# Optimization experiments

Hardware: AMD Instinct MI355X
Metric: run time of the kernel (lower is better)

## Reference

```python
import jax, jax.numpy as jnp
import numpy as np

B, T, C, H, L, FFN = 2, 2048, 512, 4, 4, 2048
H = 8
KD = C // H          # key_dim = head_dim (value_factor=1)
SCALE = KD ** -0.5
EPS = 1e-6


def _gelu(x):
    return jax.nn.gelu(x, approximate=False)  # keras default gelu is exact


def _ln(x):
    m = jnp.mean(x, axis=-1, keepdims=True)
    v = jnp.mean((x - m) ** 2, axis=-1, keepdims=True)
    return (x - m) / jnp.sqrt(v + EPS)


def _rotate_every_two(x):
    x1 = x[..., ::2]
    x2 = x[..., 1::2]
    return jnp.stack((-x2, x1), axis=-1).reshape(x.shape)


def _theta_shift(x, sin, cos):
    # x: [B,H,T,KD]; sin/cos: [T,KD] broadcast over B,H
    return x * cos + _rotate_every_two(x) * sin


def _rel_pos():
    half = KD // 2
    angle = 1.0 / (10000.0 ** jnp.linspace(0.0, 1.0, half))
    angle = jnp.repeat(angle, 2)                       # interleaved duplicate -> [KD]
    idx = jnp.arange(T, dtype=jnp.float32)
    sin = jnp.sin(idx[:, None] * angle[None, :])       # [T,KD]
    cos = jnp.cos(idx[:, None] * angle[None, :])
    decay = jnp.log(1.0 - 2.0 ** (-5.0 - jnp.arange(H, dtype=jnp.float32)))  # [H]
    diff = idx[:, None] - idx[None, :]                 # [T,T]
    masked = jnp.where(diff >= 0, jnp.exp(diff * decay[:, None, None]), 0.0)  # [H,T,T]
    mask = masked / jnp.sqrt(jnp.sum(masked, axis=-1, keepdims=True))
    return sin, cos, mask


def _split_heads(t):
    # [B,T,C] -> [B,H,T,KD]
    return t.reshape(B, T, H, KD).transpose(0, 2, 1, 3)


def _retention(x, Wq, bq, Wk, bk, Wv, bv, Wg, bg, Wo, bo, sin, cos, mask):
    q = _gelu(x @ Wq + bq)
    k = _gelu(x @ Wk + bk) * SCALE
    v = _gelu(x @ Wv + bv)
    g = _gelu(x @ Wg + bg)
    qr = _theta_shift(_split_heads(q), sin, cos)
    kr = _theta_shift(_split_heads(k), sin, cos)
    vr = _split_heads(v)
    qk = jnp.einsum('bhtd,bhsd->bhts', qr, kr) * mask[None]
    ssum = jnp.clip(jnp.abs(jnp.sum(qk, axis=-1, keepdims=True)), 1.0, None)
    qk = qk / (ssum + EPS)
    out = jnp.einsum('bhts,bhsd->bhtd', qk, vr)
    out = out.transpose(0, 2, 1, 3).reshape(B, T, C)
    out = _ln(out)                                     # group_norm (LayerNormalization)
    out = (g * jax.nn.sigmoid(g)) * out                # swish gate
    return _gelu(out @ Wo + bo)


def setup_inputs() -> dict:
    key = jax.random.key(0)
    ks = jax.random.split(key, 8)
    s = 0.02
    d = {'x': jax.random.normal(ks[0], (B, T, C), jnp.float32)}
    d['Wq'] = jax.random.normal(ks[1], (L, C, C), jnp.float32) * s
    d['bq'] = jnp.zeros((L, C), jnp.float32)
    d['Wk'] = jax.random.normal(ks[2], (L, C, C), jnp.float32) * s
    d['bk'] = jnp.zeros((L, C), jnp.float32)
    d['Wv'] = jax.random.normal(ks[3], (L, C, C), jnp.float32) * s
    d['bv'] = jnp.zeros((L, C), jnp.float32)
    d['Wg'] = jax.random.normal(ks[4], (L, C, C), jnp.float32) * s
    d['bg'] = jnp.zeros((L, C), jnp.float32)
    d['Wo'] = jax.random.normal(ks[5], (L, C, C), jnp.float32) * s
    d['bo'] = jnp.zeros((L, C), jnp.float32)
    d['W1'] = jax.random.normal(ks[6], (L, C, FFN), jnp.float32) * s
    d['b1'] = jnp.zeros((L, FFN), jnp.float32)
    d['W2'] = jax.random.normal(ks[7], (L, FFN, C), jnp.float32) * s
    d['b2'] = jnp.zeros((L, C), jnp.float32)
    return d


def reference(x, Wq, bq, Wk, bk, Wv, bv, Wg, bg, Wo, bo, W1, b1, W2, b2):
    sin, cos, mask = _rel_pos()
    for l in range(L):
        # pre-norm retention block (normalize_before=True, alpha=1, dropout off)
        res = x
        h = _ln(x)
        h = _retention(h, Wq[l], bq[l], Wk[l], bk[l], Wv[l], bv[l],
                       Wg[l], bg[l], Wo[l], bo[l], sin, cos, mask)
        x = res + h
        # pre-norm FFN block with internal layernorm (use_ffn_layernorm=True)
        res = x
        h = _ln(x)
        h = _gelu(h @ W1[l] + b1[l])
        h = _ln(h)
        h = _gelu(h @ W2[l] + b2[l])
        x = res + h
    return x
```

## Files before the change

### kernel.cpp

```cpp
#include <hip/hip_runtime.h>
#include <math.h>

typedef __bf16 bf16_t;
typedef __bf16 bf16x4 __attribute__((ext_vector_type(4)));
typedef __bf16 bf16x8 __attribute__((ext_vector_type(8)));
typedef float f32x4 __attribute__((ext_vector_type(4)));

#define DEV __device__ __forceinline__

constexpr int Bc = 2, Tc = 2048, Cc = 512, Hc = 8, FFNc = 2048, Lc = 4;
constexpr int Mc = Bc * Tc;
constexpr float kSCALE = 0.125f;
constexpr float kEPS = 1e-6f;

constexpr size_t OFF_WQKVG = 0;
constexpr size_t OFF_WO    = OFF_WQKVG + (size_t)Lc*2048*512*2;
constexpr size_t OFF_W1    = OFF_WO    + (size_t)Lc*512*512*2;
constexpr size_t OFF_W2    = OFF_W1    + (size_t)Lc*2048*512*2;
constexpr size_t OFF_BQKVG = OFF_W2    + (size_t)Lc*512*2048*2;
constexpr size_t OFF_TABC  = OFF_BQKVG + (size_t)Lc*2048*4;
constexpr size_t OFF_TABS  = OFF_TABC  + (size_t)Tc*32*4;
constexpr size_t OFF_HLN   = OFF_TABS  + (size_t)Tc*32*4;
constexpr size_t OFF_QKVG  = OFF_HLN   + (size_t)Mc*2048*2;
constexpr size_t OFF_QR    = OFF_QKVG  + (size_t)Mc*2048*4;
constexpr size_t OFF_KR    = OFF_QR    + (size_t)Bc*Hc*Tc*64*2;
constexpr size_t OFF_VT    = OFF_KR    + (size_t)Bc*Hc*Tc*64*2;
constexpr size_t OFF_AO    = OFF_VT    + (size_t)Bc*Hc*64*Tc*2;
constexpr size_t OFF_GATED = OFF_AO    + (size_t)Mc*512*4;

DEV float gelu_f(float x) { return 0.5f * x * (1.0f + erff(x * 0.70710678118654752f)); }

DEV void async_load16(const void* g, void* l) {
  __builtin_amdgcn_global_load_lds((const __attribute__((address_space(1))) unsigned int*)g,
                                   (__attribute__((address_space(3))) unsigned int*)l, 16, 0, 0);
}

__global__ __launch_bounds__(256) void transpose_pack_k(const float* __restrict__ src, bf16_t* __restrict__ dst,
                                                        int K, int N, size_t src_lstride, size_t dst_lstride) {
  __shared__ float tile[32][33];
  src += blockIdx.z * src_lstride;
  dst += blockIdx.z * dst_lstride;
  const int n0 = blockIdx.x * 32, k0 = blockIdx.y * 32;
  const int tx = threadIdx.x, ty = threadIdx.y;
#pragma unroll
  for (int j = 0; j < 32; j += 8) tile[ty + j][tx] = src[(size_t)(k0 + ty + j) * N + n0 + tx];
  __syncthreads();
#pragma unroll
  for (int j = 0; j < 32; j += 8) dst[(size_t)(n0 + ty + j) * K + k0 + tx] = (bf16_t)tile[tx][ty + j];
}

__global__ __launch_bounds__(256) void biaspack_k(const float* __restrict__ bq, const float* __restrict__ bk,
                                                  const float* __restrict__ bv, const float* __restrict__ bg,
                                                  float* __restrict__ outp) {
  const int tid = blockIdx.x * 256 + threadIdx.x;
  const int l = tid >> 11, n = tid & 2047;
  const float* srcs[4] = {bq, bk, bv, bg};
  outp[tid] = srcs[n >> 9][l * 512 + (n & 511)];
}

__global__ __launch_bounds__(256) void trig_k(float* __restrict__ tc, float* __restrict__ ts) {
  const int tid = blockIdx.x * 256 + threadIdx.x;
  const int t = tid >> 5, i = tid & 31;
  const float angle = powf(10000.f, -(float)i / 31.f);
  const float a = (float)t * angle;
  tc[tid] = cosf(a);
  ts[tid] = sinf(a);
}

template <int NC>
__global__ __launch_bounds__(256) void ln_k(const float* __restrict__ in, bf16_t* __restrict__ out) {
  constexpr int PT = NC / 256;
  const int row = blockIdx.x;
  const float* rp = in + (size_t)row * NC;
  float v[PT], s = 0.f, sq = 0.f;
#pragma unroll
  for (int i = 0; i < PT; ++i) { v[i] = rp[threadIdx.x + i * 256]; s += v[i]; sq += v[i] * v[i]; }
#pragma unroll
  for (int m = 1; m < 64; m <<= 1) { s += __shfl_xor(s, m); sq += __shfl_xor(sq, m); }
  __shared__ float red[8];
  const int wave = threadIdx.x >> 6, lane = threadIdx.x & 63;
  if (lane == 0) { red[wave] = s; red[4 + wave] = sq; }
  __syncthreads();
  s = red[0] + red[1] + red[2] + red[3];
  sq = red[4] + red[5] + red[6] + red[7];
  const float mean = s * (1.f / NC);
  const float inv = rsqrtf(sq * (1.f / NC) - mean * mean + kEPS);
  bf16_t* op = out + (size_t)row * NC;
#pragma unroll
  for (int i = 0; i < PT; ++i) op[threadIdx.x + i * 256] = (bf16_t)((v[i] - mean) * inv);
}

template <int BM, int BN, int WM, int WN, int EPI>
__global__ __launch_bounds__(256) void gemm_k(const bf16_t* __restrict__ A, const bf16_t* __restrict__ Bt,
                                              const float* __restrict__ bias, const float* __restrict__ res,
                                              float* __restrict__ out, int M, int N, int K,
                                              const float* __restrict__ tabc, const float* __restrict__ tabs,
                                              bf16_t* __restrict__ qrp, bf16_t* __restrict__ krp,
                                              bf16_t* __restrict__ vtp) {
  constexpr int BK = 32;
  constexpr int WIN_M = WM / 16, WIN_N = WN / 16;
  __shared__ bf16_t lds[2][(BM + BN) * BK];
  const int wave = threadIdx.x >> 6, lane = threadIdx.x & 63;
  const int nwg = gridDim.x * gridDim.y;
  const int orig = blockIdx.y * gridDim.x + blockIdx.x;
  const int wg = (orig & 7) * (nwg >> 3) + (orig >> 3);
  const int bx = wg % gridDim.x, by = wg / gridDim.x;
  const int m0 = by * BM, n0 = bx * BN;
  const int wm = wave >> 1, wn = wave & 1;
  f32x4 acc[WIN_M][WIN_N] = {};
  const int lrow = lane >> 2, lcb = (lane & 3) * 8;
  const int ksub = (lane >> 4) * 8, rsub = lane & 15;

#define GSTAGE(bf_, kt_)                                                              \
  {                                                                                   \
    for (int i = wave; i < BM / 16; i += 4)                                           \
      async_load16(A + (size_t)(m0 + i * 16 + lrow) * K + (kt_) + lcb,                \
                   &lds[bf_][i * 16 * BK]);                                           \
    for (int i = wave; i < BN / 16; i += 4)                                           \
      async_load16(Bt + (size_t)(n0 + i * 16 + lrow) * K + (kt_) + lcb,               \
                   &lds[bf_][BM * BK + i * 16 * BK]);                                 \
  }

  int buf = 0;
  GSTAGE(0, 0);
  __syncthreads();
  for (int kt = 0; kt < K; kt += BK) {
    if (kt + BK < K) GSTAGE(buf ^ 1, kt + BK);
    const bf16_t* bufA = &lds[buf][0];
    const bf16_t* bufB = &lds[buf][BM * BK];
    bf16x8 af[WIN_M], bfr[WIN_N];
#pragma unroll
    for (int mi = 0; mi < WIN_M; ++mi) af[mi] = *(const bf16x8*)&bufA[(wm * WM + mi * 16 + rsub) * BK + ksub];
#pragma unroll
    for (int ni = 0; ni < WIN_N; ++ni) bfr[ni] = *(const bf16x8*)&bufB[(wn * WN + ni * 16 + rsub) * BK + ksub];
#pragma unroll
    for (int mi = 0; mi < WIN_M; ++mi)
#pragma unroll
      for (int ni = 0; ni < WIN_N; ++ni)
        acc[mi][ni] = __builtin_amdgcn_mfma_f32_16x16x32_bf16(af[mi], bfr[ni], acc[mi][ni], 0, 0, 0);
    __syncthreads();
    buf ^= 1;
  }
#undef GSTAGE

#pragma unroll
  for (int mi = 0; mi < WIN_M; ++mi)
#pragma unroll
    for (int ni = 0; ni < WIN_N; ++ni) {
      const int col = n0 + wn * WN + ni * 16 + (lane & 15);
      const int row0 = m0 + wm * WM + mi * 16 + (lane >> 4) * 4;
      const float bv = bias ? bias[col] : 0.f;
      if constexpr (EPI == 2) {
        const int region = col >> 9;
        if (region <= 1) {
          const int hh = (col >> 6) & 7, d = col & 63, ti = d >> 1;
          bf16_t* dst = region ? krp : qrp;
#pragma unroll
          for (int r = 0; r < 4; ++r) {
            float v = gelu_f(acc[mi][ni][r] + bv);
            if (region == 1) v *= kSCALE;
            const float p = __shfl_xor(v, 1);
            const int m = row0 + r, t = m & 2047, bb = m >> 11;
            const float cv = tabc[t * 32 + ti], sv = tabs[t * 32 + ti];
            const float rot = (d & 1) ? p : -p;
            dst[((size_t)((bb * 8 + hh) * 2048 + t)) * 64 + d] = (bf16_t)(v * cv + rot * sv);
          }
        } else if (region == 2) {
          const int hh = (col >> 6) & 7, d = col & 63;
          const int m = row0, t0 = m & 2047, bb = m >> 11;
          bf16x4 pk;
#pragma unroll
          for (int r = 0; r < 4; ++r) pk[r] = (bf16_t)gelu_f(acc[mi][ni][r] + bv);
          *(bf16x4*)&vtp[((size_t)((bb * 8 + hh) * 64 + d)) * 2048 + t0] = pk;
        } else {
#pragma unroll
          for (int r = 0; r < 4; ++r)
            out[(size_t)(row0 + r) * N + col] = gelu_f(acc[mi][ni][r] + bv);
        }
      } else {
#pragma unroll
        for (int r = 0; r < 4; ++r) {
          float v = gelu_f(acc[mi][ni][r] + bv);
          if constexpr (EPI == 3) v += res[(size_t)(row0 + r) * N + col];
          out[(size_t)(row0 + r) * N + col] = v;
        }
      }
    }
}

__global__ __launch_bounds__(512) void retention_k(const bf16_t* __restrict__ qr, const bf16_t* __restrict__ kr,
                                                   const bf16_t* __restrict__ vt, float* __restrict__ ao) {
  const int bid = blockIdx.x;
  const int j = bid >> 3;
  const int bh = (bid & 7) * 2 + (j & 1);
  const int qp = j >> 1;
  const int h = bh & 7, b = bh >> 3;
  const int wave = threadIdx.x >> 6, lane = threadIdx.x & 63;
  const int sub = wave & 3, half = wave >> 2;
  const int gi = lane >> 4, li = lane & 15;
  const float dec = log1pf(-exp2f(-5.f - (float)h));
  const float d2 = dec * 1.44269504088896340736f;
  const float inv1md = exp2f(5.f + (float)h);
  __shared__ bf16_t kv[2][2][2][64][64];
  __shared__ bf16_t sS[8][16][76];
  __shared__ float red[4][64][21];
  const size_t base = (size_t)bh * (size_t)Tc * 64;
  const bf16_t* vbh = vt + (size_t)bh * 64 * Tc;

  const int srow = lane >> 3;
  const int schunk = (lane & 7) ^ srow;
  const int roff0 = li * 64 + (((gi) ^ (li & 7)) << 3);
  const int roff1 = li * 64 + (((gi + 4) ^ (li & 7)) << 3);

  float bS[4];
#pragma unroll
  for (int sc = 0; sc < 4; ++sc) bS[sc] = exp2f(-d2 * (float)(sc * 16 + li));

#define STAGE(bf_, st_)                                                                   \
  {                                                                                       \
    const bf16_t* kt_ = kr + base + (size_t)(st_) * 64 * 64;                              \
    const bf16_t* vt_ = vbh + (st_) * 64;                                                 \
    _Pragma("unroll") for (int jj = 0; jj < 2; ++jj) {                                    \
      const int rb_ = sub * 2 + jj;                                                       \
      async_load16(kt_ + (size_t)(rb_ * 8 + srow) * 64 + schunk * 8, &kv[bf_][half][0][rb_ * 8][0]); \
      async_load16(vt_ + (size_t)(rb_ * 8 + srow) * Tc + schunk * 8, &kv[bf_][half][1][rb_ * 8][0]); \
    }                                                                                     \
  }

  for (int part = 0; part < 2; ++part) {
    const int q = part ? (31 - qp) : qp;
    const int tw = q * 64 + sub * 16;
    bf16x8 qf0, qf1;
    {
      const bf16_t* qptr = qr + base + (size_t)(tw + li) * 64 + gi * 8;
      qf0 = *(const bf16x8*)qptr;
      qf1 = *(const bf16x8*)(qptr + 32);
    }
    f32x4 accv[4] = {};
    float rs[4] = {0.f, 0.f, 0.f, 0.f};

    const int nsteps = (q + 2) >> 1;
    int buf = 0;
    if (half <= q) STAGE(0, half);
    __syncthreads();
    for (int i = 0; i < nsteps; ++i) {
      const int st = 2 * i + half;
      const int stn = st + 2;
      if (stn <= q) STAGE(buf ^ 1, stn);
      if (st <= q) {
        const int s0g = st * 64;
        const bf16_t* kb = &kv[buf][half][0][0][0];
        const bf16_t* vb = &kv[buf][half][1][0][0];
        float aT[4];
#pragma unroll
        for (int r = 0; r < 4; ++r) aT[r] = exp2f(d2 * (float)(tw + gi * 4 + r - s0g));
#pragma unroll
        for (int sc = 0; sc < 4; ++sc) {
          const bf16x8 kf0 = *(const bf16x8*)(kb + sc * 16 * 64 + roff0);
          const bf16x8 kf1 = *(const bf16x8*)(kb + sc * 16 * 64 + roff1);
          f32x4 Sv = {};
          Sv = __builtin_amdgcn_mfma_f32_16x16x32_bf16(qf0, kf0, Sv, 0, 0, 0);
          Sv = __builtin_amdgcn_mfma_f32_16x16x32_bf16(qf1, kf1, Sv, 0, 0, 0);
          const int s_l = sc * 16 + li;
#pragma unroll
          for (int r = 0; r < 4; ++r) {
            const float w = (s0g + s_l <= tw + gi * 4 + r) ? aT[r] * bS[sc] : 0.f;
            const float val = Sv[r] * w;
            rs[r] += val;
            sS[wave][gi * 4 + r][s_l] = (bf16_t)val;
          }
        }
        const bf16x8 pa0 = *(const bf16x8*)&sS[wave][li][gi * 8];
        const bf16x8 pa1 = *(const bf16x8*)&sS[wave][li][32 + gi * 8];
#pragma unroll
        for (int dd = 0; dd < 4; ++dd) {
          const bf16x8 vb0 = *(const bf16x8*)(vb + dd * 16 * 64 + roff0);
          const bf16x8 vb1 = *(const bf16x8*)(vb + dd * 16 * 64 + roff1);
          accv[dd] = __builtin_amdgcn_mfma_f32_16x16x32_bf16(pa0, vb0, accv[dd], 0, 0, 0);
          accv[dd] = __builtin_amdgcn_mfma_f32_16x16x32_bf16(pa1, vb1, accv[dd], 0, 0, 0);
        }
      }
      __syncthreads();
      buf ^= 1;
    }

#pragma unroll
    for (int r = 0; r < 4; ++r) {
      float v = rs[r];
      v += __shfl_xor(v, 1); v += __shfl_xor(v, 2); v += __shfl_xor(v, 4); v += __shfl_xor(v, 8);
      rs[r] = v;
    }
    if (half == 1) {
      float* rp = red[sub][lane];
#pragma unroll
      for (int dd = 0; dd < 4; ++dd)
#pragma unroll
        for (int r = 0; r < 4; ++r) rp[dd * 4 + r] = accv[dd][r];
#pragma unroll
      for (int r = 0; r < 4; ++r) rp[16 + r] = rs[r];
    }
    __syncthreads();
    if (half == 0) {
      const float* rp = red[sub][lane];
#pragma unroll
      for (int r = 0; r < 4; ++r) {
        const int t = tw + gi * 4 + r;
        const float Ssum = -expm1f(dec * (float)(t + 1)) * inv1md;
        const float rt = rsqrtf(Ssum);
        const float rsv = rs[r] + rp[16 + r];
        const float den = fmaxf(fabsf(rsv * rt), 1.0f) + kEPS;
        const float scl = rt / den;
        float* op = ao + ((size_t)(b * Tc + t)) * Cc + h * 64 + li;
#pragma unroll
        for (int dd = 0; dd < 4; ++dd) op[dd * 16] = (accv[dd][r] + rp[dd * 4 + r]) * scl;
      }
    }
    __syncthreads();
  }
#undef STAGE
}

__global__ __launch_bounds__(256) void postret_k(const float* __restrict__ ao, const float* __restrict__ qkvg,
                                                 bf16_t* __restrict__ gated) {
  const int row = blockIdx.x;
  const float* rp = ao + (size_t)row * 512;
  float v0 = rp[threadIdx.x], v1 = rp[threadIdx.x + 256];
  float s = v0 + v1, sq = v0 * v0 + v1 * v1;
#pragma unroll
  for (int m = 1; m < 64; m <<= 1) { s += __shfl_xor(s, m); sq += __shfl_xor(sq, m); }
  __shared__ float red[8];
  const int wave = threadIdx.x >> 6, lane = threadIdx.x & 63;
  if (lane == 0) { red[wave] = s; red[4 + wave] = sq; }
  __syncthreads();
  s = red[0] + red[1] + red[2] + red[3];
  sq = red[4] + red[5] + red[6] + red[7];
  const float mean = s * (1.f / 512.f);
  const float inv = rsqrtf(sq * (1.f / 512.f) - mean * mean + kEPS);
  const float* gp = qkvg + (size_t)row * 2048 + 1536;
  const float g0 = gp[threadIdx.x], g1 = gp[threadIdx.x + 256];
  bf16_t* op = gated + (size_t)row * 512;
  op[threadIdx.x] = (bf16_t)(g0 / (1.f + expf(-g0)) * (v0 - mean) * inv);
  op[threadIdx.x + 256] = (bf16_t)(g1 / (1.f + expf(-g1)) * (v1 - mean) * inv);
}

extern "C" void kernel_launch(void* const* d_in, const int* in_sizes, int n_in,
                              void* d_out, int out_size, void* d_ws, size_t ws_size,
                              hipStream_t stream) {
  const float* x_in = (const float*)d_in[0];
  const float* Wq = (const float*)d_in[1];
  const float* bq = (const float*)d_in[2];
  const float* Wk = (const float*)d_in[3];
  const float* bk = (const float*)d_in[4];
  const float* Wv = (const float*)d_in[5];
  const float* bv = (const float*)d_in[6];
  const float* Wg = (const float*)d_in[7];
  const float* bg = (const float*)d_in[8];
  const float* Wo = (const float*)d_in[9];
  const float* bo = (const float*)d_in[10];
  const float* W1 = (const float*)d_in[11];
  const float* b1 = (const float*)d_in[12];
  const float* W2 = (const float*)d_in[13];
  const float* b2 = (const float*)d_in[14];

  char* ws = (char*)d_ws;
  bf16_t* WQKVG = (bf16_t*)(ws + OFF_WQKVG);
  bf16_t* WOt   = (bf16_t*)(ws + OFF_WO);
  bf16_t* W1t   = (bf16_t*)(ws + OFF_W1);
  bf16_t* W2t   = (bf16_t*)(ws + OFF_W2);
  float*  BQKVG = (float*)(ws + OFF_BQKVG);
  float*  TABC  = (float*)(ws + OFF_TABC);
  float*  TABS  = (float*)(ws + OFF_TABS);
  bf16_t* HLN   = (bf16_t*)(ws + OFF_HLN);
  float*  QKVG  = (float*)(ws + OFF_QKVG);
  bf16_t* QR    = (bf16_t*)(ws + OFF_QR);
  bf16_t* KR    = (bf16_t*)(ws + OFF_KR);
  bf16_t* VT    = (bf16_t*)(ws + OFF_VT);
  float*  AO    = (float*)(ws + OFF_AO);
  bf16_t* GATED = (bf16_t*)(ws + OFF_GATED);
  float*  xbuf  = (float*)d_out;

  hipMemcpyAsync(xbuf, x_in, (size_t)Mc * Cc * 4, hipMemcpyDeviceToDevice, stream);

  const dim3 tb(32, 8);
  const float* wsrc[4] = {Wq, Wk, Wv, Wg};
  for (int c = 0; c < 4; ++c)
    transpose_pack_k<<<dim3(Cc / 32, Cc / 32, Lc), tb, 0, stream>>>(
        wsrc[c], WQKVG + (size_t)c * Cc * Cc, Cc, Cc, (size_t)Cc * Cc, (size_t)2048 * Cc);
  transpose_pack_k<<<dim3(Cc / 32, Cc / 32, Lc), tb, 0, stream>>>(
      Wo, WOt, Cc, Cc, (size_t)Cc * Cc, (size_t)Cc * Cc);
  transpose_pack_k<<<dim3(FFNc / 32, Cc / 32, Lc), tb, 0, stream>>>(
      W1, W1t, Cc, FFNc, (size_t)Cc * FFNc, (size_t)FFNc * Cc);
  transpose_pack_k<<<dim3(Cc / 32, FFNc / 32, Lc), tb, 0, stream>>>(
      W2, W2t, FFNc, Cc, (size_t)FFNc * Cc, (size_t)Cc * FFNc);
  biaspack_k<<<32, 256, 0, stream>>>(bq, bk, bv, bg, BQKVG);
  trig_k<<<256, 256, 0, stream>>>(TABC, TABS);

  for (int l = 0; l < Lc; ++l) {
    ln_k<512><<<Mc, 256, 0, stream>>>(xbuf, HLN);
    gemm_k<64, 128, 32, 64, 2><<<dim3(2048 / 128, Mc / 64), 256, 0, stream>>>(
        HLN, WQKVG + (size_t)l * 2048 * 512, BQKVG + l * 2048, nullptr, QKVG, Mc, 2048, 512,
        TABC, TABS, QR, KR, VT);
    retention_k<<<256, 512, 0, stream>>>(QR, KR, VT, AO);
    postret_k<<<Mc, 256, 0, stream>>>(AO, QKVG, GATED);
    gemm_k<64, 64, 32, 32, 3><<<dim3(512 / 64, Mc / 64), 256, 0, stream>>>(
        GATED, WOt + (size_t)l * 512 * 512, bo + l * 512, xbuf, xbuf, Mc, 512, 512,
        nullptr, nullptr, nullptr, nullptr, nullptr);
    ln_k<512><<<Mc, 256, 0, stream>>>(xbuf, HLN);
    gemm_k<64, 128, 32, 64, 1><<<dim3(2048 / 128, Mc / 64), 256, 0, stream>>>(
        HLN, W1t + (size_t)l * 2048 * 512, b1 + l * 2048, nullptr, QKVG, Mc, 2048, 512,
        nullptr, nullptr, nullptr, nullptr, nullptr);
    ln_k<2048><<<Mc, 256, 0, stream>>>(QKVG, HLN);
    gemm_k<64, 64, 32, 32, 3><<<dim3(512 / 64, Mc / 64), 256, 0, stream>>>(
        HLN, W2t + (size_t)l * 512 * 2048, b2 + l * 512, xbuf, xbuf, Mc, 512, 2048,
        nullptr, nullptr, nullptr, nullptr, nullptr);
  }
}
```

Measured before the change: 696.5 us.

## Use triple-buffered LDS with vmcnt waits and single barrier per k-step

Switches the GEMM and retention main loops from double-buffered LDS with two __syncthreads per step to a three-slot ring. Each step issues the next tile's async loads unconditionally (clamped to a valid tile), then uses s_waitcnt vmcnt(N) plus one s_barrier so only the current tile must have landed. The goal is to cut barrier count and keep global-to-LDS loads in flight across the MFMA work. It costs 50% more LDS, which may lower occupancy, and adds redundant loads at the tail; correctness depends on the vmcnt count matching the number of loads each wave issues per stage.

Measured after the change: 675.7 us. 1.03x faster.

```diff
diff --git a/kernel.cpp b/kernel.cpp
--- a/kernel.cpp
+++ b/kernel.cpp
@@ -35,6 +35,11 @@
                                    (__attribute__((address_space(3))) unsigned int*)l, 16, 0, 0);
 }
 
+#define PIPE_WAIT_BARRIER(J_)                                        \
+  asm volatile("s_waitcnt vmcnt(%0)" ::"i"(J_) : "memory");          \
+  __builtin_amdgcn_s_barrier();                                      \
+  __builtin_amdgcn_sched_barrier(0);
+
 __global__ __launch_bounds__(256) void transpose_pack_k(const float* __restrict__ src, bf16_t* __restrict__ dst,
                                                         int K, int N, size_t src_lstride, size_t dst_lstride) {
   __shared__ float tile[32][33];
@@ -99,7 +104,8 @@
                                               bf16_t* __restrict__ vtp) {
   constexpr int BK = 32;
   constexpr int WIN_M = WM / 16, WIN_N = WN / 16;
-  __shared__ bf16_t lds[2][(BM + BN) * BK];
+  constexpr int JL = (BM + BN) / 64;
+  __shared__ bf16_t lds[3][(BM + BN) * BK];
   const int wave = threadIdx.x >> 6, lane = threadIdx.x & 63;
   const int nwg = gridDim.x * gridDim.y;
   const int orig = blockIdx.y * gridDim.x + blockIdx.x;
@@ -121,13 +127,14 @@
                    &lds[bf_][BM * BK + i * 16 * BK]);                                 \
   }
 
-  int buf = 0;
+  const int NT = K / BK;
   GSTAGE(0, 0);
-  __syncthreads();
-  for (int kt = 0; kt < K; kt += BK) {
-    if (kt + BK < K) GSTAGE(buf ^ 1, kt + BK);
-    const bf16_t* bufA = &lds[buf][0];
-    const bf16_t* bufB = &lds[buf][BM * BK];
+  for (int tt = 0; tt < NT; ++tt) {
+    const int ktn = (tt + 1 < NT) ? (tt + 1) * BK : (NT - 1) * BK;
+    GSTAGE((tt + 1) % 3, ktn);
+    PIPE_WAIT_BARRIER(JL);
+    const bf16_t* bufA = &lds[tt % 3][0];
+    const bf16_t* bufB = &lds[tt % 3][BM * BK];
     bf16x8 af[WIN_M], bfr[WIN_N];
 #pragma unroll
     for (int mi = 0; mi < WIN_M; ++mi) af[mi] = *(const bf16x8*)&bufA[(wm * WM + mi * 16 + rsub) * BK + ksub];
@@ -138,10 +145,9 @@
 #pragma unroll
       for (int ni = 0; ni < WIN_N; ++ni)
         acc[mi][ni] = __builtin_amdgcn_mfma_f32_16x16x32_bf16(af[mi], bfr[ni], acc[mi][ni], 0, 0, 0);
-    __syncthreads();
-    buf ^= 1;
   }
 #undef GSTAGE
+  asm volatile("s_waitcnt vmcnt(0)" ::: "memory");
 
 #pragma unroll
   for (int mi = 0; mi < WIN_M; ++mi)
@@ -201,7 +207,7 @@
   const float dec = log1pf(-exp2f(-5.f - (float)h));
   const float d2 = dec * 1.44269504088896340736f;
   const float inv1md = exp2f(5.f + (float)h);
-  __shared__ bf16_t kv[2][2][2][64][64];
+  __shared__ bf16_t kv[3][2][2][64][64];
   __shared__ bf16_t sS[8][16][76];
   __shared__ float red[4][64][21];
   const size_t base = (size_t)bh * (size_t)Tc * 64;
@@ -240,17 +246,17 @@
     float rs[4] = {0.f, 0.f, 0.f, 0.f};
 
     const int nsteps = (q + 2) >> 1;
-    int buf = 0;
-    if (half <= q) STAGE(0, half);
-    __syncthreads();
+    STAGE(0, (half <= q ? half : 0));
     for (int i = 0; i < nsteps; ++i) {
       const int st = 2 * i + half;
-      const int stn = st + 2;
-      if (stn <= q) STAGE(buf ^ 1, stn);
+      const int stn0 = st + 2;
+      const int stn = (stn0 <= 31) ? stn0 : 31;
+      STAGE((i + 1) % 3, stn);
+      PIPE_WAIT_BARRIER(4);
       if (st <= q) {
         const int s0g = st * 64;
-        const bf16_t* kb = &kv[buf][half][0][0][0];
-        const bf16_t* vb = &kv[buf][half][1][0][0];
+        const bf16_t* kb = &kv[i % 3][half][0][0][0];
+        const bf16_t* vb = &kv[i % 3][half][1][0][0];
         float aT[4];
 #pragma unroll
         for (int r = 0; r < 4; ++r) aT[r] = exp2f(d2 * (float)(tw + gi * 4 + r - s0g));
@@ -280,8 +286,6 @@
           accv[dd] = __builtin_amdgcn_mfma_f32_16x16x32_bf16(pa1, vb1, accv[dd], 0, 0, 0);
         }
       }
-      __syncthreads();
-      buf ^= 1;
     }
 
 #pragma unroll
```
